# Performance work log

Measured on AMD Instinct MI355X. Metric: run time of the kernel, lower is better.

The kernel has to match this reference:

```python
import jax, jax.numpy as jnp
from jax import lax
import numpy as np

B, C, H, W, D = 4, 128, 32, 32, 32
NH = 4                 # num_heads (4*NH == 16 fc input channels)
DH = C // NH           # head dim = 32
N = H * W * D          # input_size = 32768
PROJ = 64              # proj_size
EPS = 1e-12


def setup_inputs() -> dict:
    key = jax.random.key(0)
    ks = jax.random.split(key, 12)
    s = 0.02
    return {
        "x": jax.random.normal(ks[0], (B, C, H, W, D), jnp.float32),
        "Wqkvv": jax.random.normal(ks[1], (4 * C, C), jnp.float32) * s,   # qkv_bias=False
        "W_fc": jax.random.normal(ks[2], (16, 4 * NH), jnp.float32) * s,  # Conv2d 1x1
        "b_fc": jnp.zeros((16,), jnp.float32),
        "W_dep": jax.random.normal(ks[3], (C, 16, 3, 3, 3), jnp.float32) * 0.05,  # groups=DH -> in/grp=16
        "b_dep": jnp.zeros((C,), jnp.float32),
        "W_E": jax.random.normal(ks[4], (PROJ, N), jnp.float32) * s,  # E = F (shared weights)
        "b_E": jnp.zeros((PROJ,), jnp.float32),
        "temperature": jnp.ones((NH, 1, 1), jnp.float32),
        "temperature2": jnp.ones((NH, 1, 1), jnp.float32),
        "rate": jnp.full((1,), 0.5, jnp.float32),
        "rate2": jnp.full((1,), 0.5, jnp.float32),
        "W_out": jax.random.normal(ks[5], (C // 2, C), jnp.float32) * s,
        "b_out": jnp.zeros((C // 2,), jnp.float32),
        "W_out2": jax.random.normal(ks[6], (C // 2, C), jnp.float32) * s,
        "b_out2": jnp.zeros((C // 2,), jnp.float32),
    }


def _l2norm(t):
    return t / jnp.maximum(jnp.linalg.norm(t, axis=-1, keepdims=True), EPS)


def reference(x, Wqkvv, W_fc, b_fc, W_dep, b_dep, W_E, b_E,
              temperature, temperature2, rate, rate2,
              W_out, b_out, W_out2, b_out2):
    Bc, Cc, Hc, Wc, Dc = x.shape
    Nc = Hc * Wc * Dc
    # tokens: [B, N, C]
    xf = jnp.transpose(x, (0, 2, 3, 4, 1)).reshape(Bc, Nc, Cc)
    qkvv = xf @ Wqkvv.T  # [B, N, 4C]

    # ---- fused grouped-conv branch ----
    f_all = jnp.transpose(qkvv.reshape(Bc, Nc, 4 * NH, DH), (0, 2, 1, 3))  # [B,16,N,DH]
    f = jnp.einsum('oi,bind->bond', W_fc, f_all) + b_fc[None, :, None, None]  # 1x1 conv
    f_conv = jnp.transpose(f, (0, 3, 1, 2)).reshape(Bc, 16 * DH, Hc, Wc, Dc)
    out_conv = lax.conv_general_dilated(
        f_conv, W_dep, window_strides=(1, 1, 1), padding='SAME',
        dimension_numbers=('NCDHW', 'OIDHW', 'NCDHW'), feature_group_count=DH)
    out_conv = out_conv + b_dep[None, :, None, None, None]
    out_conv = jnp.transpose(out_conv, (0, 2, 3, 4, 1)).reshape(Bc, Nc, Cc)

    # ---- dual attention ----
    qkvv5 = jnp.transpose(qkvv.reshape(Bc, Nc, 4, NH, DH), (2, 0, 3, 1, 4))  # [4,B,nh,N,dh]
    q = jnp.swapaxes(qkvv5[0], -2, -1)    # [B,nh,dh,N]
    k = jnp.swapaxes(qkvv5[1], -2, -1)
    v_CA = jnp.swapaxes(qkvv5[2], -2, -1)
    v_SA = jnp.swapaxes(qkvv5[3], -2, -1)

    k_proj = k @ W_E.T + b_E              # [B,nh,dh,proj]  (E)
    v_SA_proj = v_SA @ W_E.T + b_E        # shared weights   (F)

    qn = _l2norm(q)
    kn = _l2norm(k)

    # channel attention: [B,nh,dh,dh]
    attn_CA = jax.nn.softmax(jnp.einsum('bhdn,bhen->bhde', qn, kn) * temperature, axis=-1)
    x_CA = jnp.transpose(attn_CA @ v_CA, (0, 3, 1, 2)).reshape(Bc, Nc, Cc)  # [B,N,C]

    # spatial (Linformer-style) attention: [B,nh,N,proj]
    attn_SA = jax.nn.softmax(
        jnp.einsum('bhdn,bhdp->bhnp', qn, k_proj) * temperature2, axis=-1)
    x_SA = jnp.einsum('bhnp,bhdp->bhnd', attn_SA, v_SA_proj)  # [B,nh,N,dh]
    x_SA = jnp.transpose(x_SA, (0, 3, 1, 2)).reshape(Bc, Nc, Cc)  # faithful to torch permute

    x_SA = x_SA @ W_out.T + b_out    # [B,N,C/2]
    x_CA = x_CA @ W_out2.T + b_out2  # [B,N,C/2]
    x_attn = jnp.concatenate([x_SA, x_CA], axis=-1)
    return rate * x_attn + rate2 * out_conv
```

## Files before the change

kernel.cpp:

```cpp
#include <hip/hip_runtime.h>
#include <hip/hip_bf16.h>

typedef unsigned short u16;
typedef __attribute__((ext_vector_type(8))) short bf16x8;
typedef __attribute__((ext_vector_type(4))) float f32x4;

#define MFMA16(a,b,c) __builtin_amdgcn_mfma_f32_16x16x32_bf16((a),(b),(c),0,0,0)

__device__ __forceinline__ float bf2f(u16 u){ union{unsigned int i; float f;} v; v.i=((unsigned int)u)<<16; return v.f; }
__device__ __forceinline__ u16 f2bf(float f){ union{float f; unsigned int i;} v; v.f=f; unsigned int r=v.i+0x7fffu+((v.i>>16)&1u); return (u16)(r>>16); }
__device__ __forceinline__ unsigned int pk2(float a, float b){
  __hip_bfloat162 h = __float22bfloat162_rn(make_float2(a,b));
  union{ __hip_bfloat162 h; unsigned int u; } v; v.h = h; return v.u;
}

__global__ __launch_bounds__(256) void kcvt3(const float* __restrict__ WE, u16* __restrict__ WEb,
                                             const float* __restrict__ Wq, u16* __restrict__ Wqb,
                                             const float* __restrict__ Wo, u16* __restrict__ Wob){
  int bid = blockIdx.x;
  const float* src; u16* dst; int base;
  if(bid < 2048){ src = WE; dst = WEb; base = bid*1024; }
  else if(bid < 2112){ src = Wq; dst = Wqb; base = (bid-2048)*1024; }
  else { src = Wo; dst = Wob; base = (bid-2112)*1024; }
  int i = base + threadIdx.x*4;
  float4 v = *(const float4*)(src + i);
  ushort4 o; o.x = f2bf(v.x); o.y = f2bf(v.y); o.z = f2bf(v.z); o.w = f2bf(v.w);
  *(ushort4*)(dst + i) = o;
}

#define K1PAD 136
__global__ __launch_bounds__(256) void k1_qkvv(const float* __restrict__ x, const u16* __restrict__ Wqb, u16* __restrict__ qkvvT){
  __shared__ u16 lB[128*K1PAD];
  const int tile = blockIdx.x;
  const int b  = tile >> 8;
  const int n0 = (tile & 255) << 7;
  const int tid = threadIdx.x;
  const float* xb = x + (size_t)b*128*32768;
  {
    const int cb = (tid >> 4) << 1;
    const int m  = tid & 15;
    const int t8 = m << 3;
    const int swz = (m & 3) << 3;
    unsigned int* basep = (unsigned int*)lB;
    #pragma unroll
    for(int r=0;r<4;++r){
      const int c = cb + (r<<5);
      const float4* p0 = (const float4*)(xb + (size_t)c*32768 + n0 + t8);
      const float4* p1 = (const float4*)(xb + (size_t)(c+1)*32768 + n0 + t8);
      float4 a0 = p0[0], a1 = p0[1];
      float4 b0 = p1[0], b1 = p1[1];
      const int rot = (swz + c) & 127;
      int di = t8*68 + (rot>>1);
      basep[di      ] = pk2(a0.x, b0.x);
      basep[di+  68 ] = pk2(a0.y, b0.y);
      basep[di+ 136 ] = pk2(a0.z, b0.z);
      basep[di+ 204 ] = pk2(a0.w, b0.w);
      basep[di+ 272 ] = pk2(a1.x, b1.x);
      basep[di+ 340 ] = pk2(a1.y, b1.y);
      basep[di+ 408 ] = pk2(a1.z, b1.z);
      basep[di+ 476 ] = pk2(a1.w, b1.w);
    }
  }
  __syncthreads();
  const int wave = tid >> 6, lane = tid & 63;
  const int wm = (wave & 1) << 6;
  const int wn = (wave >> 1) << 6;
  const int lm = lane & 15, lq = lane >> 4;
  u16* outb = qkvvT + (size_t)b*512*32768;
  for(int s=0;s<4;++s){
    const int oc0 = s << 7;
    f32x4 acc[4][4] = {};
    const u16* Arow = Wqb + (oc0 + wm + lm)*128 + lq*8;
    #pragma unroll
    for(int ks=0; ks<4; ++ks){
      bf16x8 af[4], bfr[4];
      #pragma unroll
      for(int mt=0;mt<4;++mt) af[mt] = *(const bf16x8*)(Arow + mt*2048 + ks*32);
      #pragma unroll
      for(int nt=0;nt<4;++nt){
        const int tr = wn + nt*16 + lm;
        const int rot = ((((tr>>3)&3)<<3) + ks*32 + lq*8) & 127;
        bfr[nt] = *(const bf16x8*)(&lB[tr*K1PAD + rot]);
      }
      #pragma unroll
      for(int mt=0;mt<4;++mt)
        #pragma unroll
        for(int nt=0;nt<4;++nt)
          acc[mt][nt] = MFMA16(af[mt], bfr[nt], acc[mt][nt]);
    }
    #pragma unroll
    for(int mt=0;mt<4;++mt){
      const int ocr = oc0 + wm + mt*16 + lq*4;
      #pragma unroll
      for(int nt=0;nt<4;++nt){
        const int n = n0 + wn + nt*16 + lm;
        #pragma unroll
        for(int r=0;r<4;++r) outb[(size_t)(ocr+r)*32768 + n] = f2bf(acc[mt][nt][r]);
      }
    }
  }
}

__global__ void k2_weff(const float* __restrict__ Wdep, const float* __restrict__ Wfc,
                        const float* __restrict__ bdep, const float* __restrict__ bfc,
                        float* __restrict__ W_eff, float* __restrict__ bias_eff){
  int idx = blockIdx.x*256 + threadIdx.x;
  if(idx < 55296){
    int ol = idx & 3;
    int k  = (idx >> 2) % 27;
    int j  = (idx / 108) & 15;
    int g  = idx / 1728;
    int oc = g*4 + ol;
    float s = 0.f;
    for(int o=0;o<16;++o) s += Wdep[(oc*16 + o)*27 + k] * Wfc[o*16 + j];
    W_eff[idx] = s;
  }
  if(idx < 128){
    float s = bdep[idx];
    for(int o=0;o<16;++o){
      float wsum = 0.f;
      for(int k=0;k<27;++k) wsum += Wdep[(idx*16 + o)*27 + k];
      s += wsum * bfc[o];
    }
    bias_eff[idx] = s;
  }
}

__global__ __launch_bounds__(256) void k2b_norms(const u16* __restrict__ qkvvT, float* __restrict__ invn){
  const int b = blockIdx.x >> 8, c = blockIdx.x & 255;
  const u16* row = qkvvT + ((size_t)b*512 + c)*32768;
  float s = 0.f;
  for(int n = threadIdx.x*8; n < 32768; n += 2048){
    bf16x8 v = *(const bf16x8*)(row + n);
    #pragma unroll
    for(int j=0;j<8;++j){ float f = bf2f((u16)v[j]); s += f*f; }
  }
  for(int off=32; off; off>>=1) s += __shfl_down(s, off, 64);
  __shared__ float wsum[4];
  if((threadIdx.x & 63)==0) wsum[threadIdx.x>>6] = s;
  __syncthreads();
  if(threadIdx.x==0){
    float t = wsum[0]+wsum[1]+wsum[2]+wsum[3];
    invn[blockIdx.x] = 1.0f / fmaxf(sqrtf(t), 1e-12f);
  }
}

__global__ __launch_bounds__(256) void k3_proj(const u16* __restrict__ qkvvT, const u16* __restrict__ WEb,
                                               float* __restrict__ kp, float* __restrict__ vp){
  const int kc = blockIdx.x;
  const int b  = blockIdx.y;
  const int ts = blockIdx.z >> 1;
  const int rh = (blockIdx.z & 1) << 6;
  const int wave = threadIdx.x >> 6, lane = threadIdx.x & 63;
  const int lm = lane & 15, lq = lane >> 4;
  const int coff = ts ? 384 : 128;
  const u16* Arow = qkvvT + ((size_t)b*512 + coff + rh + wave*16 + lm)*32768 + kc*1024 + lq*8;
  f32x4 acc[4] = {};
  for(int ks=0; ks<32; ++ks){
    bf16x8 af = *(const bf16x8*)(Arow + ks*32);
    #pragma unroll
    for(int nt=0;nt<4;++nt){
      bf16x8 bfr = *(const bf16x8*)(WEb + (size_t)(nt*16 + lm)*32768 + kc*1024 + ks*32 + lq*8);
      acc[nt] = MFMA16(af, bfr, acc[nt]);
    }
  }
  float* out = (ts ? vp : kp) + (size_t)b*128*64;
  const int r0 = rh + wave*16 + lq*4;
  #pragma unroll
  for(int nt=0;nt<4;++nt){
    const int p = nt*16 + lm;
    #pragma unroll
    for(int r=0;r<4;++r) atomicAdd(&out[(r0+r)*64 + p], acc[nt][r]);
  }
}

__global__ __launch_bounds__(64) void k4_gram(const u16* __restrict__ qkvvT, float* __restrict__ G){
  const int kc = blockIdx.x, b = blockIdx.y, h = blockIdx.z;
  const int lane = threadIdx.x, lm = lane & 15, lq = lane >> 4;
  const u16* qb = qkvvT + ((size_t)b*512 + h*32)*32768 + kc*512 + lq*8;
  const u16* kb = qb + (size_t)128*32768;
  f32x4 acc[2][2] = {};
  for(int ks=0; ks<16; ++ks){
    bf16x8 af[2], bfr[2];
    af[0]  = *(const bf16x8*)(qb + (size_t)lm*32768 + ks*32);
    af[1]  = *(const bf16x8*)(qb + (size_t)(16+lm)*32768 + ks*32);
    bfr[0] = *(const bf16x8*)(kb + (size_t)lm*32768 + ks*32);
    bfr[1] = *(const bf16x8*)(kb + (size_t)(16+lm)*32768 + ks*32);
    #pragma unroll
    for(int mt=0;mt<2;++mt)
      #pragma unroll
      for(int nt=0;nt<2;++nt) acc[mt][nt] = MFMA16(af[mt], bfr[nt], acc[mt][nt]);
  }
  float* Gb = G + (size_t)(b*4 + h)*1024;
  #pragma unroll
  for(int mt=0;mt<2;++mt)
    #pragma unroll
    for(int nt=0;nt<2;++nt)
      #pragma unroll
      for(int r=0;r<4;++r){
        int d = mt*16 + lq*4 + r, e = nt*16 + lm;
        atomicAdd(&Gb[d*32 + e], acc[mt][nt][r]);
      }
}

__global__ __launch_bounds__(256) void k4b_softmax_m2(const float* __restrict__ G, const float* __restrict__ invn,
                                                      const float* __restrict__ temp, const float* __restrict__ Wout2,
                                                      u16* __restrict__ M2){
  const int b = blockIdx.x >> 2, h = blockIdx.x & 3;
  __shared__ float A[32][33];
  const float* Gb = G + (size_t)(b*4 + h)*1024;
  const float* inb = invn + b*256;
  const float th = temp[h];
  const int tid = threadIdx.x;
  if(tid < 32){
    const int d = tid;
    const float iq = inb[h*32 + d];
    float row[32]; float mx = -1e30f;
    #pragma unroll
    for(int e=0;e<32;++e){
      float v = Gb[d*32+e] * iq * inb[128 + h*32 + e] * th;
      row[e] = v; mx = fmaxf(mx, v);
    }
    float s = 0.f;
    #pragma unroll
    for(int e=0;e<32;++e){ float ee = __expf(row[e]-mx); row[e] = ee; s += ee; }
    const float rs = 1.0f/s;
    #pragma unroll
    for(int e=0;e<32;++e) A[d][e] = row[e]*rs;
  }
  __syncthreads();
  for(int o = tid; o < 2048; o += 256){
    const int j = o >> 5, e = o & 31;
    float s = 0.f;
    #pragma unroll
    for(int d=0;d<32;++d) s += Wout2[j*128 + h*32 + d] * A[d][e];
    M2[((size_t)b*64 + j)*128 + h*32 + e] = f2bf(s);
  }
}

__global__ __launch_bounds__(256) void k5_xsa(const u16* __restrict__ qkvvT, const float* __restrict__ kp,
                                              const float* __restrict__ vp, const float* __restrict__ invn,
                                              const float* __restrict__ bE, const float* __restrict__ temp2,
                                              u16* __restrict__ xsa){
  const int b = blockIdx.z, h = blockIdx.y, n0 = blockIdx.x*256;
  __shared__ float lkp[32][64], lvp[32][64], liq[32];
  const int tid = threadIdx.x;
  for(int o = tid; o < 2048; o += 256){
    int d = o >> 6, p = o & 63;
    float be = bE[p];
    size_t base = ((size_t)b*128 + h*32 + d)*64 + p;
    lkp[d][p] = kp[base] + be;
    lvp[d][p] = vp[base] + be;
  }
  if(tid < 32) liq[tid] = invn[b*256 + h*32 + tid];
  __syncthreads();
  const int n = n0 + tid;
  const u16* qb = qkvvT + ((size_t)b*512 + h*32)*32768 + n;
  const float t2 = temp2[h];
  float s[64];
  #pragma unroll
  for(int p=0;p<64;++p) s[p]=0.f;
  for(int d=0; d<32; ++d){
    float qv = bf2f(qb[(size_t)d*32768]) * liq[d];
    #pragma unroll
    for(int p=0;p<64;++p) s[p] += qv * lkp[d][p];
  }
  float mx = -1e30f;
  #pragma unroll
  for(int p=0;p<64;++p){ s[p] *= t2; mx = fmaxf(mx, s[p]); }
  float sum = 0.f;
  #pragma unroll
  for(int p=0;p<64;++p){ s[p] = __expf(s[p]-mx); sum += s[p]; }
  const float r = 1.0f/sum;
  u16* ob = xsa + (((size_t)b*4 + h)*32)*32768 + n;
  for(int d=0; d<32; ++d){
    float acc = 0.f;
    #pragma unroll
    for(int p=0;p<64;++p) acc += s[p]*lvp[d][p];
    ob[(size_t)d*32768] = f2bf(acc*r);
  }
}

#define CSX 36
#define CSZ 360
__global__ __launch_bounds__(256,6) void kconv(const u16* __restrict__ qkvvT, const float* __restrict__ W_eff,
                                               const float* __restrict__ bias_eff, u16* __restrict__ convo){
  __shared__ float lf[10*CSZ];
  const int zt = blockIdx.x >> 2, yt = blockIdx.x & 3;
  const int g = blockIdx.y, b = blockIdx.z;
  const int tid = threadIdx.x;
  const int z0 = zt << 3, y0 = yt << 3;
  const int lz = tid >> 5;
  const int vy = (tid >> 2) & 7;
  const int x0 = (tid & 3) << 3;
  float acc[4][8];
  #pragma unroll
  for(int oc=0;oc<4;++oc)
    #pragma unroll
    for(int xi=0;xi<8;++xi) acc[oc][xi] = 0.f;
  const u16* qb = qkvvT + (size_t)b*512*32768;
  const int sz = tid / 10, sy = tid - sz*10;
  const int gz = z0 + sz - 1, gy = y0 + sy - 1;
  const bool srow_ok = (tid < 100) && ((unsigned)gz < 32u) && ((unsigned)gy < 32u);
  float2* d2 = (float2*)&lf[sz*CSZ + sy*CSX];
  const float* Wgbase = W_eff + (size_t)(g*16)*108;

  for(int p=0;p<16;++p){
    __syncthreads();
    if(tid < 100){
      if(srow_ok){
        const u16* src = qb + ((size_t)(p*32 + g))*32768 + gz*1024 + gy*32;
        float carry = 0.f;
        #pragma unroll
        for(int q=0;q<4;++q){
          bf16x8 v = *(const bf16x8*)(src + q*8);
          float w0=bf2f((u16)v[0]), w1=bf2f((u16)v[1]), w2=bf2f((u16)v[2]), w3=bf2f((u16)v[3]);
          float w4=bf2f((u16)v[4]), w5=bf2f((u16)v[5]), w6=bf2f((u16)v[6]), w7=bf2f((u16)v[7]);
          d2[q*4+0] = make_float2(carry, w0);
          d2[q*4+1] = make_float2(w1, w2);
          d2[q*4+2] = make_float2(w3, w4);
          d2[q*4+3] = make_float2(w5, w6);
          carry = w7;
        }
        d2[16] = make_float2(carry, 0.f);
      } else {
        #pragma unroll
        for(int i=0;i<17;++i) d2[i] = make_float2(0.f, 0.f);
      }
    }
    __syncthreads();
    const float* Wg = Wgbase + p*108;
    #pragma unroll
    for(int dy=0;dy<3;++dy){
      #pragma unroll
      for(int dz=0;dz<3;++dz){
        const float* row = &lf[(lz+dz)*CSZ + (vy+dy)*CSX + x0];
        float4 fa = *(const float4*)(row);
        float4 fb = *(const float4*)(row+4);
        float2 fc = *(const float2*)(row+8);
        float fw[10] = {fa.x,fa.y,fa.z,fa.w, fb.x,fb.y,fb.z,fb.w, fc.x,fc.y};
        const float* Wb = Wg + (dz*3+dy)*12;
        #pragma unroll
        for(int kx=0;kx<3;++kx){
          float4 wv = *(const float4*)(Wb + kx*4);
          #pragma unroll
          for(int xi=0;xi<8;++xi){
            float f = fw[xi+kx];
            acc[0][xi] += wv.x*f; acc[1][xi] += wv.y*f;
            acc[2][xi] += wv.z*f; acc[3][xi] += wv.w*f;
          }
        }
      }
    }
  }
  const float4 bi = *(const float4*)(bias_eff + g*4);
  const int nb = (z0 + lz)*1024 + (y0+vy)*32 + x0;
  u16* ob = convo + ((size_t)b*32768 + nb)*128 + g*4;
  #pragma unroll
  for(int xi=0;xi<8;++xi){
    unsigned long long pk = (unsigned long long)f2bf(acc[0][xi] + bi.x)
                          | ((unsigned long long)f2bf(acc[1][xi] + bi.y) << 16)
                          | ((unsigned long long)f2bf(acc[2][xi] + bi.z) << 32)
                          | ((unsigned long long)f2bf(acc[3][xi] + bi.w) << 48);
    *(unsigned long long*)(ob + (size_t)xi*128) = pk;
  }
}

#define K6PAD 136
__global__ __launch_bounds__(256) void k6_out(const u16* __restrict__ qkvvT, const u16* __restrict__ xsa,
                                              const u16* __restrict__ conv, const u16* __restrict__ M2,
                                              const u16* __restrict__ Woutb, const float* __restrict__ bout,
                                              const float* __restrict__ bout2, const float* __restrict__ rate,
                                              const float* __restrict__ rate2, float* __restrict__ out){
  __shared__ u16 lA[128*K6PAD];
  const int tile = blockIdx.x;
  const int b  = tile >> 8;
  const int n0 = (tile & 255) << 7;
  const int tid = threadIdx.x;
  const int hh = (n0 >> 8) & 3;
  const int dh = n0 >> 10;
  const u16* xseg = xsa + (((size_t)b*4 + hh)*32 + dh)*32768 + ((size_t)(n0 & 255) << 7);
  {
    const int r = tid >> 1, off = (tid & 1) << 6;
    const u16* src = xseg + r*128 + off;
    u16* dst = &lA[r*K6PAD + off];
    #pragma unroll
    for(int q=0;q<8;++q) *(bf16x8*)(dst + q*8) = *(const bf16x8*)(src + q*8);
  }
  __syncthreads();
  const int wave = tid >> 6, lane = tid & 63;
  const int lm = lane & 15, lq = lane >> 4;
  f32x4 accS[2][4] = {};
  #pragma unroll
  for(int ks=0;ks<4;++ks){
    bf16x8 a0 = *(const bf16x8*)(&lA[(wave*32 + lm)*K6PAD + ks*32 + lq*8]);
    bf16x8 a1 = *(const bf16x8*)(&lA[(wave*32 + 16 + lm)*K6PAD + ks*32 + lq*8]);
    #pragma unroll
    for(int nt=0;nt<4;++nt){
      bf16x8 bw = *(const bf16x8*)(Woutb + (nt*16 + lm)*128 + ks*32 + lq*8);
      accS[0][nt] = MFMA16(a0, bw, accS[0][nt]);
      accS[1][nt] = MFMA16(a1, bw, accS[1][nt]);
    }
  }
  __syncthreads();
  {
    const int cb = tid >> 4, t8 = (tid & 15) << 3;
    const u16* vb = qkvvT + ((size_t)b*512 + 256)*32768 + n0;
    #pragma unroll
    for(int r2=0;r2<8;++r2){
      int c = cb + (r2<<4);
      bf16x8 v = *(const bf16x8*)(vb + (size_t)c*32768 + t8);
      #pragma unroll
      for(int j=0;j<8;++j) lA[(t8+j)*K6PAD + c] = (u16)v[j];
    }
  }
  __syncthreads();
  f32x4 accC[2][4] = {};
  #pragma unroll
  for(int ks=0;ks<4;++ks){
    bf16x8 a0 = *(const bf16x8*)(&lA[(wave*32 + lm)*K6PAD + ks*32 + lq*8]);
    bf16x8 a1 = *(const bf16x8*)(&lA[(wave*32 + 16 + lm)*K6PAD + ks*32 + lq*8]);
    #pragma unroll
    for(int nt=0;nt<4;++nt){
      bf16x8 bm = *(const bf16x8*)(M2 + ((size_t)b*64 + nt*16 + lm)*128 + ks*32 + lq*8);
      accC[0][nt] = MFMA16(a0, bm, accC[0][nt]);
      accC[1][nt] = MFMA16(a1, bm, accC[1][nt]);
    }
  }
  const float rt = rate[0], rt2 = rate2[0];
  float* ob = out + ((size_t)b*32768 + n0)*128;
  const u16* cbp = conv + ((size_t)b*32768 + n0)*128;
  #pragma unroll
  for(int mt=0;mt<2;++mt){
    #pragma unroll
    for(int r=0;r<4;++r){
      const int tok = wave*32 + mt*16 + lq*4 + r;
      #pragma unroll
      for(int nt=0;nt<4;++nt){
        const int j = nt*16 + lm;
        float sa = accS[mt][nt][r] + bout[j];
        float ca = accC[mt][nt][r] + bout2[j];
        float c1 = bf2f(cbp[(size_t)tok*128 + j]);
        float c2 = bf2f(cbp[(size_t)tok*128 + 64 + j]);
        ob[(size_t)tok*128 + j]      = rt*sa + rt2*c1;
        ob[(size_t)tok*128 + 64 + j] = rt*ca + rt2*c2;
      }
    }
  }
}

extern "C" void kernel_launch(void* const* d_in, const int* in_sizes, int n_in,
                              void* d_out, int out_size, void* d_ws, size_t ws_size,
                              hipStream_t stream){
  const float* x     = (const float*)d_in[0];
  const float* Wq    = (const float*)d_in[1];
  const float* Wfc   = (const float*)d_in[2];
  const float* bfc   = (const float*)d_in[3];
  const float* Wdep  = (const float*)d_in[4];
  const float* bdep  = (const float*)d_in[5];
  const float* WE    = (const float*)d_in[6];
  const float* bE    = (const float*)d_in[7];
  const float* temp  = (const float*)d_in[8];
  const float* temp2 = (const float*)d_in[9];
  const float* rate  = (const float*)d_in[10];
  const float* rate2 = (const float*)d_in[11];
  const float* Wout  = (const float*)d_in[12];
  const float* bout  = (const float*)d_in[13];
  const float* Wout2 = (const float*)d_in[14];
  const float* bout2 = (const float*)d_in[15];
  float* outp = (float*)d_out;

  char* w = (char*)d_ws;
  size_t off = 0;
  auto alloc = [&](size_t bytes)->char*{ char* p = w + off; off += (bytes + 255) & ~(size_t)255; return p; };
  u16*   qkvvT  = (u16*)  alloc((size_t)4*512*32768*2);
  u16*   xsa    = (u16*)  alloc((size_t)4*4*32*32768*2);
  u16*   convb  = (u16*)  alloc((size_t)4*32768*128*2);
  float* W_eff  = (float*)alloc(55296*4);
  float* biasef = (float*)alloc(128*4);
  float* invn   = (float*)alloc(1024*4);
  float* kp     = (float*)alloc(32768*4);
  float* vp     = (float*)alloc(32768*4);
  float* G      = (float*)alloc(16384*4);
  u16*   M2     = (u16*)  alloc(32768*2);
  u16*   WEb    = (u16*)  alloc((size_t)2097152*2);
  u16*   Wqb    = (u16*)  alloc(65536*2);
  u16*   Woutb  = (u16*)  alloc(8192*2);

  hipMemsetAsync(kp, 0, (size_t)(32768+32768+16384)*4, stream);

  kcvt3         <<<2120,          256, 0, stream>>>(WE, WEb, Wq, Wqb, Wout, Woutb);
  k1_qkvv       <<<1024,          256, 0, stream>>>(x, Wqb, qkvvT);
  k2_weff       <<<216,           256, 0, stream>>>(Wdep, Wfc, bdep, bfc, W_eff, biasef);
  k2b_norms     <<<1024,          256, 0, stream>>>(qkvvT, invn);
  k3_proj       <<<dim3(32,4,4),  256, 0, stream>>>(qkvvT, WEb, kp, vp);
  k4_gram       <<<dim3(64,4,4),   64, 0, stream>>>(qkvvT, G);
  k4b_softmax_m2<<<16,            256, 0, stream>>>(G, invn, temp, Wout2, M2);
  k5_xsa        <<<dim3(128,4,4), 256, 0, stream>>>(qkvvT, kp, vp, invn, bE, temp2, xsa);
  kconv         <<<dim3(16,32,4), 256, 0, stream>>>(qkvvT, W_eff, biasef, convb);
  k6_out        <<<1024,          256, 0, stream>>>(qkvvT, xsa, convb, M2, Woutb, bout, bout2, rate, rate2, outp);
}
```

Baseline: 624.7 us.

## Fuse q/k norm reduction into QKV GEMM epilogue and simplify spatial attention kernel

The QKV projection kernel now accumulates per-channel sums of squares for q and k in its epilogue, using wave shuffles and atomics. This replaces the separate norm kernel that re-read 256 channels per batch of the bf16 qkvv buffer, and a tiny kernel turns the sums into inverse norms. The spatial attention kernel drops its shared-memory staging of kp/vp and instead reads them directly as float4 (uniform, cache-resident). It folds the b_E bias algebraically through qsum and a post-softmax bias term. Trade-offs: atomics add contention, norms are now computed from fp32 accumulators rather than rounded bf16 values, and the direct global reads depend on cache behaviour.

```diff
diff --git a/kernel.cpp b/kernel.cpp
--- a/kernel.cpp
+++ b/kernel.cpp
@@ -29,7 +29,8 @@
 }
 
 #define K1PAD 136
-__global__ __launch_bounds__(256) void k1_qkvv(const float* __restrict__ x, const u16* __restrict__ Wqb, u16* __restrict__ qkvvT){
+__global__ __launch_bounds__(256) void k1_qkvv(const float* __restrict__ x, const u16* __restrict__ Wqb,
+                                               u16* __restrict__ qkvvT, float* __restrict__ sumsq){
   __shared__ u16 lB[128*K1PAD];
   const int tile = blockIdx.x;
   const int b  = tile >> 8;
@@ -98,6 +99,20 @@
         for(int r=0;r<4;++r) outb[(size_t)(ocr+r)*32768 + n] = f2bf(acc[mt][nt][r]);
       }
     }
+    if(s < 2){
+      const int cbase = b*256 + oc0 + wm;
+      #pragma unroll
+      for(int mt=0;mt<4;++mt){
+        #pragma unroll
+        for(int r=0;r<4;++r){
+          float ss = acc[mt][0][r]*acc[mt][0][r] + acc[mt][1][r]*acc[mt][1][r]
+                   + acc[mt][2][r]*acc[mt][2][r] + acc[mt][3][r]*acc[mt][3][r];
+          ss += __shfl_xor(ss, 1); ss += __shfl_xor(ss, 2);
+          ss += __shfl_xor(ss, 4); ss += __shfl_xor(ss, 8);
+          if(lm == 0) atomicAdd(&sumsq[cbase + mt*16 + lq*4 + r], ss);
+        }
+      }
+    }
   }
 }
 
@@ -126,23 +141,9 @@
   }
 }
 
-__global__ __launch_bounds__(256) void k2b_norms(const u16* __restrict__ qkvvT, float* __restrict__ invn){
-  const int b = blockIdx.x >> 8, c = blockIdx.x & 255;
-  const u16* row = qkvvT + ((size_t)b*512 + c)*32768;
-  float s = 0.f;
-  for(int n = threadIdx.x*8; n < 32768; n += 2048){
-    bf16x8 v = *(const bf16x8*)(row + n);
-    #pragma unroll
-    for(int j=0;j<8;++j){ float f = bf2f((u16)v[j]); s += f*f; }
-  }
-  for(int off=32; off; off>>=1) s += __shfl_down(s, off, 64);
-  __shared__ float wsum[4];
-  if((threadIdx.x & 63)==0) wsum[threadIdx.x>>6] = s;
-  __syncthreads();
-  if(threadIdx.x==0){
-    float t = wsum[0]+wsum[1]+wsum[2]+wsum[3];
-    invn[blockIdx.x] = 1.0f / fmaxf(sqrtf(t), 1e-12f);
-  }
+__global__ __launch_bounds__(256) void k2c_invn(const float* __restrict__ sumsq, float* __restrict__ invn){
+  int i = blockIdx.x*256 + threadIdx.x;
+  invn[i] = 1.0f / fmaxf(sqrtf(sumsq[i]), 1e-12f);
 }
 
 __global__ __launch_bounds__(256) void k3_proj(const u16* __restrict__ qkvvT, const u16* __restrict__ WEb,
@@ -243,40 +244,59 @@
                                               const float* __restrict__ bE, const float* __restrict__ temp2,
                                               u16* __restrict__ xsa){
   const int b = blockIdx.z, h = blockIdx.y, n0 = blockIdx.x*256;
-  __shared__ float lkp[32][64], lvp[32][64], liq[32];
   const int tid = threadIdx.x;
-  for(int o = tid; o < 2048; o += 256){
-    int d = o >> 6, p = o & 63;
-    float be = bE[p];
-    size_t base = ((size_t)b*128 + h*32 + d)*64 + p;
-    lkp[d][p] = kp[base] + be;
-    lvp[d][p] = vp[base] + be;
-  }
-  if(tid < 32) liq[tid] = invn[b*256 + h*32 + tid];
-  __syncthreads();
   const int n = n0 + tid;
   const u16* qb = qkvvT + ((size_t)b*512 + h*32)*32768 + n;
+  const float* iqp = invn + b*256 + h*32;
+  const float* kpb = kp + ((size_t)b*128 + h*32)*64;
+  const float* vpb = vp + ((size_t)b*128 + h*32)*64;
   const float t2 = temp2[h];
   float s[64];
   #pragma unroll
   for(int p=0;p<64;++p) s[p]=0.f;
+  float qsum = 0.f;
   for(int d=0; d<32; ++d){
-    float qv = bf2f(qb[(size_t)d*32768]) * liq[d];
-    #pragma unroll
-    for(int p=0;p<64;++p) s[p] += qv * lkp[d][p];
-  }
+    const float qv = bf2f(qb[(size_t)d*32768]) * iqp[d];
+    qsum += qv;
+    const float4* row = (const float4*)(kpb + d*64);
+    #pragma unroll
+    for(int p4=0;p4<16;++p4){
+      float4 w = row[p4];
+      s[p4*4+0] += qv*w.x; s[p4*4+1] += qv*w.y;
+      s[p4*4+2] += qv*w.z; s[p4*4+3] += qv*w.w;
+    }
+  }
+  const float4* be4 = (const float4*)bE;
   float mx = -1e30f;
   #pragma unroll
-  for(int p=0;p<64;++p){ s[p] *= t2; mx = fmaxf(mx, s[p]); }
+  for(int p4=0;p4<16;++p4){
+    float4 be = be4[p4];
+    float v0 = (s[p4*4+0] + qsum*be.x)*t2;
+    float v1 = (s[p4*4+1] + qsum*be.y)*t2;
+    float v2 = (s[p4*4+2] + qsum*be.z)*t2;
+    float v3 = (s[p4*4+3] + qsum*be.w)*t2;
+    s[p4*4+0]=v0; s[p4*4+1]=v1; s[p4*4+2]=v2; s[p4*4+3]=v3;
+    mx = fmaxf(mx, fmaxf(fmaxf(v0,v1), fmaxf(v2,v3)));
+  }
   float sum = 0.f;
   #pragma unroll
   for(int p=0;p<64;++p){ s[p] = __expf(s[p]-mx); sum += s[p]; }
   const float r = 1.0f/sum;
+  float pb = 0.f;
+  #pragma unroll
+  for(int p4=0;p4<16;++p4){
+    float4 be = be4[p4];
+    pb += s[p4*4+0]*be.x + s[p4*4+1]*be.y + s[p4*4+2]*be.z + s[p4*4+3]*be.w;
+  }
   u16* ob = xsa + (((size_t)b*4 + h)*32)*32768 + n;
   for(int d=0; d<32; ++d){
-    float acc = 0.f;
-    #pragma unroll
-    for(int p=0;p<64;++p) acc += s[p]*lvp[d][p];
+    const float4* row = (const float4*)(vpb + d*64);
+    float acc = pb;
+    #pragma unroll
+    for(int p4=0;p4<16;++p4){
+      float4 w = row[p4];
+      acc += s[p4*4+0]*w.x + s[p4*4+1]*w.y + s[p4*4+2]*w.z + s[p4*4+3]*w.w;
+    }
     ob[(size_t)d*32768] = f2bf(acc*r);
   }
 }
@@ -482,17 +502,18 @@
   float* kp     = (float*)alloc(32768*4);
   float* vp     = (float*)alloc(32768*4);
   float* G      = (float*)alloc(16384*4);
+  float* sumsq  = (float*)alloc(1024*4);
   u16*   M2     = (u16*)  alloc(32768*2);
   u16*   WEb    = (u16*)  alloc((size_t)2097152*2);
   u16*   Wqb    = (u16*)  alloc(65536*2);
   u16*   Woutb  = (u16*)  alloc(8192*2);
 
-  hipMemsetAsync(kp, 0, (size_t)(32768+32768+16384)*4, stream);
+  hipMemsetAsync(kp, 0, (size_t)(32768+32768+16384+1024)*4, stream);
 
   kcvt3         <<<2120,          256, 0, stream>>>(WE, WEb, Wq, Wqb, Wout, Woutb);
-  k1_qkvv       <<<1024,          256, 0, stream>>>(x, Wqb, qkvvT);
+  k1_qkvv       <<<1024,          256, 0, stream>>>(x, Wqb, qkvvT, sumsq);
+  k2c_invn      <<<4,             256, 0, stream>>>(sumsq, invn);
   k2_weff       <<<216,           256, 0, stream>>>(Wdep, Wfc, bdep, bfc, W_eff, biasef);
-  k2b_norms     <<<1024,          256, 0, stream>>>(qkvvT, invn);
   k3_proj       <<<dim3(32,4,4),  256, 0, stream>>>(qkvvT, WEb, kp, vp);
   k4_gram       <<<dim3(64,4,4),   64, 0, stream>>>(qkvvT, G);
   k4b_softmax_m2<<<16,            256, 0, stream>>>(G, invn, temp, Wout2, M2);
```

Result: slower. 720.1 us (+15.3%).

## Rewrite spatial attention kernel with bf16 MFMA using split hi/lo precision

Applied to the files above, without the earlier changes.

The k5_xsa kernel moves from per-thread scalar FP32 dot products over 64 projections to wave-level 16x16x32 bf16 MFMA tiles for both the score and output matmuls. Operands are split into bf16 hi and lo parts (three MFMAs for scores, two for output) to keep close to FP32 accuracy. The softmax is reduced across lanes with shuffles and the probabilities are staged through LDS. This removes the large per-thread register arrays and the scalar FMA work. It adds extra MFMA passes and LDS traffic, and rounding the probabilities to bf16 adds some error.

```diff
diff --git a/kernel.cpp b/kernel.cpp
--- a/kernel.cpp
+++ b/kernel.cpp
@@ -242,42 +242,108 @@
                                               const float* __restrict__ vp, const float* __restrict__ invn,
                                               const float* __restrict__ bE, const float* __restrict__ temp2,
                                               u16* __restrict__ xsa){
-  const int b = blockIdx.z, h = blockIdx.y, n0 = blockIdx.x*256;
-  __shared__ float lkp[32][64], lvp[32][64], liq[32];
+  __shared__ __align__(16) u16 L[14336];
+  __shared__ float liqt[32];
+  u16* lkAh = L;
+  u16* lkAl = L + 2560;
+  u16* lvAh = L + 5120;
+  u16* lvAl = L + 7424;
+  u16* Pl   = L + 9728;
+  const int b = blockIdx.z, h = blockIdx.y;
   const int tid = threadIdx.x;
-  for(int o = tid; o < 2048; o += 256){
-    int d = o >> 6, p = o & 63;
-    float be = bE[p];
-    size_t base = ((size_t)b*128 + h*32 + d)*64 + p;
-    lkp[d][p] = kp[base] + be;
-    lvp[d][p] = vp[base] + be;
-  }
-  if(tid < 32) liq[tid] = invn[b*256 + h*32 + tid];
-  __syncthreads();
-  const int n = n0 + tid;
-  const u16* qb = qkvvT + ((size_t)b*512 + h*32)*32768 + n;
   const float t2 = temp2[h];
-  float s[64];
-  #pragma unroll
-  for(int p=0;p<64;++p) s[p]=0.f;
-  for(int d=0; d<32; ++d){
-    float qv = bf2f(qb[(size_t)d*32768]) * liq[d];
-    #pragma unroll
-    for(int p=0;p<64;++p) s[p] += qv * lkp[d][p];
-  }
-  float mx = -1e30f;
-  #pragma unroll
-  for(int p=0;p<64;++p){ s[p] *= t2; mx = fmaxf(mx, s[p]); }
-  float sum = 0.f;
-  #pragma unroll
-  for(int p=0;p<64;++p){ s[p] = __expf(s[p]-mx); sum += s[p]; }
-  const float r = 1.0f/sum;
-  u16* ob = xsa + (((size_t)b*4 + h)*32)*32768 + n;
-  for(int d=0; d<32; ++d){
-    float acc = 0.f;
-    #pragma unroll
-    for(int p=0;p<64;++p) acc += s[p]*lvp[d][p];
-    ob[(size_t)d*32768] = f2bf(acc*r);
+  {
+    const int p = tid >> 2, d8 = (tid & 3) << 3;
+    const float be = bE[p];
+    const float* kpb = kp + ((size_t)b*128 + h*32)*64;
+    #pragma unroll
+    for(int j=0;j<8;++j){
+      float v = kpb[(size_t)(d8+j)*64 + p] + be;
+      u16 hi = f2bf(v);
+      lkAh[p*40 + d8 + j] = hi;
+      lkAl[p*40 + d8 + j] = f2bf(v - bf2f(hi));
+    }
+  }
+  {
+    const int d = tid >> 3, p8 = (tid & 7) << 3;
+    const float* vpb = vp + ((size_t)b*128 + h*32)*64;
+    #pragma unroll
+    for(int j=0;j<8;++j){
+      float v = vpb[(size_t)d*64 + p8 + j] + bE[p8+j];
+      u16 hi = f2bf(v);
+      lvAh[d*72 + p8 + j] = hi;
+      lvAl[d*72 + p8 + j] = f2bf(v - bf2f(hi));
+    }
+  }
+  if(tid < 32) liqt[tid] = invn[b*256 + h*32 + tid] * t2;
+  __syncthreads();
+  const int wave = tid >> 6, lane = tid & 63;
+  const int lm = lane & 15, lq = lane >> 4;
+  const int tokw = blockIdx.x*256 + wave*64;
+  const u16* qb = qkvvT + ((size_t)b*512 + h*32)*32768;
+  float iq[8];
+  #pragma unroll
+  for(int j=0;j<8;++j) iq[j] = liqt[lq*8+j];
+  u16* PW = Pl + wave*1152 + lm*72;
+  u16* ob = xsa + (((size_t)b*4 + h)*32)*32768;
+  for(int nt=0; nt<4; ++nt){
+    const int tok = tokw + nt*16 + lm;
+    union { u16 u[8]; bf16x8 v; } qh, ql;
+    #pragma unroll
+    for(int j=0;j<8;++j){
+      float qv = bf2f(qb[(size_t)(lq*8+j)*32768 + tok]) * iq[j];
+      u16 hi = f2bf(qv);
+      qh.u[j] = hi;
+      ql.u[j] = f2bf(qv - bf2f(hi));
+    }
+    f32x4 accS[4];
+    #pragma unroll
+    for(int mt=0;mt<4;++mt){
+      bf16x8 Ah = *(const bf16x8*)(lkAh + (mt*16+lm)*40 + lq*8);
+      bf16x8 Al = *(const bf16x8*)(lkAl + (mt*16+lm)*40 + lq*8);
+      f32x4 a = {};
+      a = MFMA16(Ah, qh.v, a);
+      a = MFMA16(Ah, ql.v, a);
+      a = MFMA16(Al, qh.v, a);
+      accS[mt] = a;
+    }
+    float mx = -1e30f;
+    #pragma unroll
+    for(int mt=0;mt<4;++mt)
+      mx = fmaxf(mx, fmaxf(fmaxf(accS[mt][0],accS[mt][1]), fmaxf(accS[mt][2],accS[mt][3])));
+    mx = fmaxf(mx, __shfl_xor(mx,16));
+    mx = fmaxf(mx, __shfl_xor(mx,32));
+    float pexp[4][4];
+    float sum = 0.f;
+    #pragma unroll
+    for(int mt=0;mt<4;++mt)
+      #pragma unroll
+      for(int r=0;r<4;++r){ float e = __expf(accS[mt][r]-mx); pexp[mt][r]=e; sum+=e; }
+    sum += __shfl_xor(sum,16);
+    sum += __shfl_xor(sum,32);
+    const float rinv = 1.0f/sum;
+    #pragma unroll
+    for(int mt=0;mt<4;++mt){
+      *(unsigned int*)(PW + mt*16 + lq*4)     = pk2(pexp[mt][0], pexp[mt][1]);
+      *(unsigned int*)(PW + mt*16 + lq*4 + 2) = pk2(pexp[mt][2], pexp[mt][3]);
+    }
+    f32x4 accO[2] = {};
+    #pragma unroll
+    for(int ks=0;ks<2;++ks){
+      bf16x8 Pb = *(const bf16x8*)(PW + ks*32 + lq*8);
+      #pragma unroll
+      for(int mt=0;mt<2;++mt){
+        bf16x8 Avh = *(const bf16x8*)(lvAh + (mt*16+lm)*72 + ks*32 + lq*8);
+        bf16x8 Avl = *(const bf16x8*)(lvAl + (mt*16+lm)*72 + ks*32 + lq*8);
+        accO[mt] = MFMA16(Avh, Pb, accO[mt]);
+        accO[mt] = MFMA16(Avl, Pb, accO[mt]);
+      }
+    }
+    #pragma unroll
+    for(int mt=0;mt<2;++mt)
+      #pragma unroll
+      for(int r=0;r<4;++r)
+        ob[(size_t)(mt*16+lq*4+r)*32768 + tok] = f2bf(accO[mt][r]*rinv);
   }
 }
 
```

Result: faster. 556.3 us (-11.0%).
